# Performance work log

Hardware: AMD Instinct MI355X
Metric: run time of the kernel (lower is better)

The kernel has to match this reference:

```python
import jax, jax.numpy as jnp
import numpy as np

N_NODES = 100000
N_EDGES = 3200000
IN_DIM = 128
HIDDEN = 128
N_GRAPHS = 64


def setup_inputs() -> dict:
    key = jax.random.key(0)
    ks = jax.random.split(key, 16)
    feat = jax.random.normal(ks[0], (N_NODES, IN_DIM), dtype=jnp.float32)
    src = jax.random.randint(ks[1], (N_EDGES,), 0, N_NODES, dtype=jnp.int32)
    dst = jax.random.randint(ks[2], (N_EDGES,), 0, N_NODES, dtype=jnp.int32)
    graph_ids = jnp.sort(jax.random.randint(ks[3], (N_NODES,), 0, N_GRAPHS, dtype=jnp.int32))
    # GraphConv weights (in_feats, out_feats) + bias, DGL default glorot-ish scale
    def lin(k, fi, fo):
        s = 1.0 / np.sqrt(fi)
        kw, kb = jax.random.split(k)
        W = jax.random.uniform(kw, (fi, fo), jnp.float32, -s, s)
        b = jax.random.uniform(kb, (fo,), jnp.float32, -s, s)
        return W, b
    W1, b1 = lin(ks[4], IN_DIM, HIDDEN)
    W2, b2 = lin(ks[5], HIDDEN, HIDDEN)
    # MLPReadout(128, 1, L=3): 128->64->32->16->1
    Wm0, bm0 = lin(ks[6], 128, 64)
    Wm1, bm1 = lin(ks[7], 64, 32)
    Wm2, bm2 = lin(ks[8], 32, 16)
    Wm3, bm3 = lin(ks[9], 16, 1)
    return dict(feat=feat, src=src, dst=dst, graph_ids=graph_ids, num_graphs=N_GRAPHS,
                W1=W1, b1=b1, W2=W2, b2=b2,
                Wm0=Wm0, bm0=bm0, Wm1=Wm1, bm1=bm1, Wm2=Wm2, bm2=bm2, Wm3=Wm3, bm3=bm3)


def reference(feat, src, dst, graph_ids, num_graphs,
              W1, b1, W2, b2,
              Wm0, bm0, Wm1, bm1, Wm2, bm2, Wm3, bm3):
    N = feat.shape[0]
    ones_e = jnp.ones(src.shape[0], dtype=feat.dtype)
    # DGL GraphConv norm='both': D_out^{-1/2} on src side, D_in^{-1/2} on dst side,
    # degrees clamped to >=1 (allow_zero_in_degree=True)
    deg_out = jnp.clip(jax.ops.segment_sum(ones_e, src, num_segments=N), 1.0)
    deg_in = jnp.clip(jax.ops.segment_sum(ones_e, dst, num_segments=N), 1.0)
    norm_src = jax.lax.rsqrt(deg_out)[:, None]  # [N,1]
    norm_dst = jax.lax.rsqrt(deg_in)[:, None]

    def gconv(h, W, b):
        h = h * norm_src
        agg = jax.ops.segment_sum(h[src], dst, num_segments=N)  # SpMM: [N,d]
        return agg * norm_dst @ W + b

    h = jax.nn.relu(gconv(feat, W1, b1))
    h = jax.nn.relu(gconv(h, W2, b2))

    # dgl.mean_nodes: per-graph mean over nodes
    counts = jnp.clip(jax.ops.segment_sum(jnp.ones(N, dtype=h.dtype), graph_ids, num_segments=num_graphs), 1.0)
    hg = jax.ops.segment_sum(h, graph_ids, num_segments=num_graphs) / counts[:, None]  # [G, hidden]

    # MLPReadout
    y = jax.nn.relu(hg @ Wm0 + bm0)
    y = jax.nn.relu(y @ Wm1 + bm1)
    y = jax.nn.relu(y @ Wm2 + bm2)
    return y @ Wm3 + bm3  # [G, 1]
```

## Files before the change

### kernel.cpp

```cpp
#include <hip/hip_runtime.h>
#include <hip/hip_fp16.h>

#define N_NODES 100000
#define N_EDGES 3200000
#define DIM 128
#define NG 64
#define GS_CHUNKS 16

#define KSH 8
#define BKT 256
#define NBKT ((N_NODES + BKT - 1) / BKT)
#define CHUNK 8192
#define NBLK ((N_EDGES + CHUNK - 1) / CHUNK)

using f16x8 = __attribute__((ext_vector_type(8))) _Float16;
using f32x4 = __attribute__((ext_vector_type(4))) float;

__global__ __launch_bounds__(256) void k_hist1(const int* __restrict__ src, const int* __restrict__ dst,
                                               int* __restrict__ histD, int* __restrict__ histS,
                                               int* __restrict__ rowtot) {
    __shared__ int hD[4 * NBKT];
    __shared__ int hS[4 * NBKT];
    int t = threadIdx.x, blk = blockIdx.x;
    int w = t >> 6;
    for (int i = t; i < 4 * NBKT; i += 256) { hD[i] = 0; hS[i] = 0; }
    __syncthreads();
    int base = blk * CHUNK;
    for (int i = t; i < CHUNK; i += 256) {
        int e = base + i;
        if (e < N_EDGES) {
            atomicAdd(&hD[w * NBKT + (dst[e] >> KSH)], 1);
            atomicAdd(&hS[w * NBKT + (src[e] >> KSH)], 1);
        }
    }
    __syncthreads();
    for (int i = t; i < NBKT; i += 256) {
        int d = hD[i] + hD[NBKT + i] + hD[2 * NBKT + i] + hD[3 * NBKT + i];
        int s = hS[i] + hS[NBKT + i] + hS[2 * NBKT + i] + hS[3 * NBKT + i];
        histD[i * NBLK + blk] = d;
        histS[i * NBLK + blk] = s;
        atomicAdd(&rowtot[i], d);
        atomicAdd(&rowtot[NBKT + i], s);
    }
}

__global__ __launch_bounds__(512) void k_rowapply(int* __restrict__ histD, int* __restrict__ histS,
                                                  const int* __restrict__ rowtot) {
    __shared__ int sh[512];
    __shared__ int red[512];
    int r = blockIdx.x;
    int half = (r < NBKT) ? 0 : 1;
    int pos = half ? (r - NBKT) : r;
    int* a = half ? (histS + (size_t)pos * NBLK) : (histD + (size_t)pos * NBLK);
    int t = threadIdx.x;
    red[t] = (t < pos) ? rowtot[half * NBKT + t] : 0;
    __syncthreads();
    for (int off = 256; off > 0; off >>= 1) {
        if (t < off) red[t] += red[t + off];
        __syncthreads();
    }
    int basev = red[0];
    int x = (t < NBLK) ? a[t] : 0;
    sh[t] = x; __syncthreads();
    for (int off = 1; off < 512; off <<= 1) {
        int y = sh[t]; int u = (t >= off) ? sh[t - off] : 0;
        __syncthreads(); sh[t] = y + u; __syncthreads();
    }
    if (t < NBLK) a[t] = sh[t] - x + basev;
}

__global__ __launch_bounds__(256) void k_scatter1(const int* __restrict__ src, const int* __restrict__ dst,
                                                  const int* __restrict__ histD, const int* __restrict__ histS,
                                                  int* __restrict__ bufD, unsigned short* __restrict__ bufS) {
    __shared__ int cD[NBKT];
    __shared__ int cS[NBKT];
    int t = threadIdx.x, blk = blockIdx.x;
    for (int i = t; i < NBKT; i += 256) {
        cD[i] = histD[i * NBLK + blk];
        cS[i] = histS[i * NBLK + blk];
    }
    __syncthreads();
    int base = blk * CHUNK;
    for (int i = t; i < CHUNK; i += 256) {
        int e = base + i;
        if (e < N_EDGES) {
            int s = src[e], d = dst[e];
            int pD = atomicAdd(&cD[d >> KSH], 1);
            bufD[pD] = ((d & (BKT - 1)) << 17) | s;
            int pS = atomicAdd(&cS[s >> KSH], 1);
            bufS[pS] = (unsigned short)(s & (BKT - 1));
        }
    }
}

__global__ __launch_bounds__(256) void k_pass2s(const unsigned short* __restrict__ bufS,
                                                const int* __restrict__ histS,
                                                float* __restrict__ norm_src) {
    __shared__ int binc[BKT];
    int b = blockIdx.x, t = threadIdx.x;
    int start = histS[b * NBLK];
    int end = (b + 1 < NBKT) ? histS[(b + 1) * NBLK] : N_EDGES;
    if (t < BKT) binc[t] = 0;
    __syncthreads();
    for (int i = start + t; i < end; i += 256) atomicAdd(&binc[bufS[i]], 1);
    __syncthreads();
    int nb = N_NODES - b * BKT; if (nb > BKT) nb = BKT;
    if (t < nb) {
        int c = binc[t]; if (c < 1) c = 1;
        norm_src[b * BKT + t] = rsqrtf((float)c);
    }
}

__global__ __launch_bounds__(256) void k_pass2(const int* __restrict__ bufD,
                                               const int* __restrict__ histD,
                                               int* __restrict__ rowptr, float* __restrict__ norm_dst,
                                               int* __restrict__ col) {
    __shared__ int binc[BKT];
    __shared__ int binoff[BKT];
    int b = blockIdx.x, t = threadIdx.x;
    int start = histD[b * NBLK];
    int end = (b + 1 < NBKT) ? histD[(b + 1) * NBLK] : N_EDGES;
    if (t < BKT) binc[t] = 0;
    __syncthreads();
    for (int i = start + t; i < end; i += 256) atomicAdd(&binc[bufD[i] >> 17], 1);
    __syncthreads();
    if (t < 64) {
        int base4 = t * 4;
        int loc[4]; int s4 = 0;
        #pragma unroll
        for (int k = 0; k < 4; k++) { loc[k] = s4; s4 += binc[base4 + k]; }
        int x = s4;
        #pragma unroll
        for (int off = 1; off < 64; off <<= 1) {
            int y = __shfl_up(x, off);
            if (t >= off) x += y;
        }
        int excl = x - s4;
        #pragma unroll
        for (int k = 0; k < 4; k++) binoff[base4 + k] = excl + loc[k];
    }
    __syncthreads();
    int nb = N_NODES - b * BKT; if (nb > BKT) nb = BKT;
    if (t < nb) {
        rowptr[b * BKT + t] = start + binoff[t];
        int c = binc[t]; if (c < 1) c = 1;
        norm_dst[b * BKT + t] = rsqrtf((float)c);
    }
    if (b == NBKT - 1 && t == 0) rowptr[N_NODES] = N_EDGES;
    __syncthreads();
    if (t < BKT) binc[t] = binoff[t];
    __syncthreads();
    for (int i = start + t; i < end; i += 256) {
        int v = bufD[i];
        int ld = v >> 17, s = v & 0x1FFFF;
        int p = atomicAdd(&binc[ld], 1);
        col[start + p] = s;
    }
}

__global__ __launch_bounds__(256) void k_cast8(const float* __restrict__ in,
                                               const float* __restrict__ norm_src,
                                               unsigned* __restrict__ out) {
    int i4 = blockIdx.x * 256 + threadIdx.x;
    const int TOT = N_NODES * DIM / 4;
    if (i4 >= TOT) return;
    int row = i4 >> 5;
    float sc = norm_src[row];
    float4 v = ((const float4*)in)[i4];
    unsigned w = 0;
    w = __builtin_amdgcn_cvt_pk_fp8_f32(v.x * sc, v.y * sc, w, 0);
    w = __builtin_amdgcn_cvt_pk_fp8_f32(v.z * sc, v.w * sc, w, 1);
    out[i4] = w;
}

#define ACC8(r) do {                                                                  \
    auto p0 = __builtin_amdgcn_cvt_pk_f32_fp8((r).x, 0); a0 += p0[0]; a1 += p0[1];    \
    auto p1 = __builtin_amdgcn_cvt_pk_f32_fp8((r).x, 1); a2 += p1[0]; a3 += p1[1];    \
    auto p2 = __builtin_amdgcn_cvt_pk_f32_fp8((r).y, 0); a4 += p2[0]; a5 += p2[1];    \
    auto p3 = __builtin_amdgcn_cvt_pk_f32_fp8((r).y, 1); a6 += p3[0]; a7 += p3[1];    \
    auto p4 = __builtin_amdgcn_cvt_pk_f32_fp8((r).z, 0); a8 += p4[0]; a9 += p4[1];    \
    auto p5 = __builtin_amdgcn_cvt_pk_f32_fp8((r).z, 1); a10 += p5[0]; a11 += p5[1];  \
    auto p6 = __builtin_amdgcn_cvt_pk_f32_fp8((r).w, 0); a12 += p6[0]; a13 += p6[1];  \
    auto p7 = __builtin_amdgcn_cvt_pk_f32_fp8((r).w, 1); a14 += p7[0]; a15 += p7[1];  \
} while (0)

__global__ __launch_bounds__(256) void k_spmm8(const unsigned char* __restrict__ in,
                       const int* __restrict__ rowptr, const int* __restrict__ col,
                       const float* __restrict__ norm_dst, __half2* __restrict__ out) {
    int wid = (blockIdx.x * 256 + threadIdx.x) >> 6;
    int lane = threadIdx.x & 63;
    int rg = lane >> 3, l8 = lane & 7;
    int node = wid * 8 + rg;
    if (node >= N_NODES) return;
    int jb = rowptr[node], je = rowptr[node + 1];
    float a0 = 0.f, a1 = 0.f, a2 = 0.f, a3 = 0.f, a4 = 0.f, a5 = 0.f, a6 = 0.f, a7 = 0.f;
    float a8 = 0.f, a9 = 0.f, a10 = 0.f, a11 = 0.f, a12 = 0.f, a13 = 0.f, a14 = 0.f, a15 = 0.f;
    int j = jb;
    for (; j + 2 <= je; j += 2) {
        int s0 = col[j], s1 = col[j + 1];
        uint4 r0 = *(const uint4*)&in[(size_t)s0 * 128 + l8 * 16];
        uint4 r1 = *(const uint4*)&in[(size_t)s1 * 128 + l8 * 16];
        ACC8(r0);
        ACC8(r1);
    }
    if (j < je) {
        int s0 = col[j];
        uint4 r0 = *(const uint4*)&in[(size_t)s0 * 128 + l8 * 16];
        ACC8(r0);
    }
    float nd = norm_dst[node];
    __half2 h0 = __floats2half2_rn(a0 * nd, a1 * nd);
    __half2 h1 = __floats2half2_rn(a2 * nd, a3 * nd);
    __half2 h2 = __floats2half2_rn(a4 * nd, a5 * nd);
    __half2 h3 = __floats2half2_rn(a6 * nd, a7 * nd);
    __half2 h4 = __floats2half2_rn(a8 * nd, a9 * nd);
    __half2 h5 = __floats2half2_rn(a10 * nd, a11 * nd);
    __half2 h6 = __floats2half2_rn(a12 * nd, a13 * nd);
    __half2 h7 = __floats2half2_rn(a14 * nd, a15 * nd);
    uint4 o0, o1;
    o0.x = *(unsigned*)&h0; o0.y = *(unsigned*)&h1;
    o0.z = *(unsigned*)&h2; o0.w = *(unsigned*)&h3;
    o1.x = *(unsigned*)&h4; o1.y = *(unsigned*)&h5;
    o1.z = *(unsigned*)&h6; o1.w = *(unsigned*)&h7;
    *(uint4*)&out[(size_t)node * 64 + l8 * 8] = o0;
    *(uint4*)&out[(size_t)node * 64 + l8 * 8 + 4] = o1;
}

template <bool SCALE, bool OUT8>
__global__ __launch_bounds__(256) void k_gemm_mfma(const __half* __restrict__ A,
        const float* __restrict__ W, const float* __restrict__ bias,
        const float* __restrict__ rowscale, void* __restrict__ outp) {
    __shared__ _Float16 lds[128 * 136];
    int tid = threadIdx.x;
    for (int idx = tid * 4; idx < DIM * DIM; idx += 256 * 4) {
        int k = idx >> 7, n = idx & 127;
        float4 w = *(const float4*)&W[idx];
        lds[(n + 0) * 136 + k] = (_Float16)w.x;
        lds[(n + 1) * 136 + k] = (_Float16)w.y;
        lds[(n + 2) * 136 + k] = (_Float16)w.z;
        lds[(n + 3) * 136 + k] = (_Float16)w.w;
    }
    __syncthreads();
    int wv = tid >> 6, lane = tid & 63;
    int rbase = blockIdx.x * 64 + wv * 16;
    int l15 = lane & 15, kg = lane >> 4;
    int arow = rbase + l15; if (arow >= N_NODES) arow = N_NODES - 1;
    const _Float16* Af = (const _Float16*)A + (size_t)arow * DIM + kg * 8;
    f16x8 a0 = *(const f16x8*)(Af + 0);
    f16x8 a1 = *(const f16x8*)(Af + 32);
    f16x8 a2 = *(const f16x8*)(Af + 64);
    f16x8 a3 = *(const f16x8*)(Af + 96);
    f32x4 acc[8];
    #pragma unroll
    for (int nt = 0; nt < 8; nt++) acc[nt] = (f32x4){0.f, 0.f, 0.f, 0.f};
    #pragma unroll
    for (int nt = 0; nt < 8; nt++) {
        const _Float16* bb = &lds[(nt * 16 + l15) * 136 + kg * 8];
        f16x8 b0 = *(const f16x8*)(bb + 0);
        f16x8 b1 = *(const f16x8*)(bb + 32);
        f16x8 b2 = *(const f16x8*)(bb + 64);
        f16x8 b3 = *(const f16x8*)(bb + 96);
        acc[nt] = __builtin_amdgcn_mfma_f32_16x16x32_f16(a0, b0, acc[nt], 0, 0, 0);
        acc[nt] = __builtin_amdgcn_mfma_f32_16x16x32_f16(a1, b1, acc[nt], 0, 0, 0);
        acc[nt] = __builtin_amdgcn_mfma_f32_16x16x32_f16(a2, b2, acc[nt], 0, 0, 0);
        acc[nt] = __builtin_amdgcn_mfma_f32_16x16x32_f16(a3, b3, acc[nt], 0, 0, 0);
    }
    __syncthreads();
    float bsc[4];
    #pragma unroll
    for (int r = 0; r < 4; r++) {
        if (SCALE) {
            int row = rbase + kg * 4 + r; if (row >= N_NODES) row = N_NODES - 1;
            bsc[r] = rowscale[row];
        } else bsc[r] = 1.f;
    }
    #pragma unroll
    for (int nt = 0; nt < 8; nt++) {
        float bv = bias[nt * 16 + l15];
        #pragma unroll
        for (int r = 0; r < 4; r++) {
            float v = fmaxf(acc[nt][r] + bv, 0.f) * bsc[r];
            lds[(size_t)(wv * 16 + kg * 4 + r) * 136 + nt * 16 + l15] = (_Float16)v;
        }
    }
    __syncthreads();
    #pragma unroll
    for (int t = 0; t < 4; t++) {
        int lrow = wv * 16 + t * 4 + kg;
        int grow = rbase + t * 4 + kg;
        f16x8 v = *(const f16x8*)&lds[(size_t)lrow * 136 + l15 * 8];
        if (grow < N_NODES) {
            if (OUT8) {
                unsigned w0 = 0, w1 = 0;
                w0 = __builtin_amdgcn_cvt_pk_fp8_f32((float)v[0], (float)v[1], w0, 0);
                w0 = __builtin_amdgcn_cvt_pk_fp8_f32((float)v[2], (float)v[3], w0, 1);
                w1 = __builtin_amdgcn_cvt_pk_fp8_f32((float)v[4], (float)v[5], w1, 0);
                w1 = __builtin_amdgcn_cvt_pk_fp8_f32((float)v[6], (float)v[7], w1, 1);
                uint2 o; o.x = w0; o.y = w1;
                *(uint2*)&((unsigned char*)outp)[(size_t)grow * 128 + l15 * 8] = o;
            } else {
                *(f16x8*)&((_Float16*)outp)[(size_t)grow * DIM + l15 * 8] = v;
            }
        }
    }
}

__global__ __launch_bounds__(256) void k_graphsum_part(const __half2* __restrict__ h,
                           const int* __restrict__ gids, float* __restrict__ partial) {
    __shared__ float redx[256];
    __shared__ float redy[256];
    __shared__ int sb[2];
    int g = blockIdx.x;
    int c = blockIdx.y;
    if (threadIdx.x == 0) {
        int lo = 0, hi = N_NODES;
        while (lo < hi) { int mid = (lo + hi) >> 1; if (gids[mid] < g) lo = mid + 1; else hi = mid; }
        sb[0] = lo;
        lo = 0; hi = N_NODES;
        while (lo < hi) { int mid = (lo + hi) >> 1; if (gids[mid] <= g) lo = mid + 1; else hi = mid; }
        sb[1] = lo;
    }
    __syncthreads();
    int s = sb[0], e = sb[1];
    int p = threadIdx.x & 63;
    int r = threadIdx.x >> 6;
    int clen = (e - s + GS_CHUNKS - 1) / GS_CHUNKS;
    int b0 = s + c * clen;
    int b1 = b0 + clen; if (b1 > e) b1 = e;
    float ax = 0.f, ay = 0.f;
    for (int nd = b0 + r; nd < b1; nd += 4) {
        float2 f = __half22float2(h[(size_t)nd * 64 + p]);
        ax += f.x; ay += f.y;
    }
    redx[threadIdx.x] = ax; redy[threadIdx.x] = ay;
    __syncthreads();
    if (threadIdx.x < 64) {
        float sx = redx[threadIdx.x] + redx[threadIdx.x + 64] + redx[threadIdx.x + 128] + redx[threadIdx.x + 192];
        float sy = redy[threadIdx.x] + redy[threadIdx.x + 64] + redy[threadIdx.x + 128] + redy[threadIdx.x + 192];
        float* pp = &partial[((size_t)g * GS_CHUNKS + c) * DIM];
        pp[2 * threadIdx.x] = sx;
        pp[2 * threadIdx.x + 1] = sy;
    }
}

__global__ __launch_bounds__(128) void k_mlp(const float* __restrict__ partial,
                      const int* __restrict__ gids,
                      const float* __restrict__ Wm0, const float* __restrict__ bm0,
                      const float* __restrict__ Wm1, const float* __restrict__ bm1,
                      const float* __restrict__ Wm2, const float* __restrict__ bm2,
                      const float* __restrict__ Wm3, const float* __restrict__ bm3,
                      float* __restrict__ out) {
    __shared__ float hb[DIM];
    __shared__ float l0[64];
    __shared__ float l1[32];
    __shared__ float l2[16];
    __shared__ int scnt;
    int g = blockIdx.x;
    int t = threadIdx.x;
    if (t == 0) {
        int lo = 0, hi = N_NODES;
        while (lo < hi) { int mid = (lo + hi) >> 1; if (gids[mid] < g) lo = mid + 1; else hi = mid; }
        int s = lo;
        lo = 0; hi = N_NODES;
        while (lo < hi) { int mid = (lo + hi) >> 1; if (gids[mid] <= g) lo = mid + 1; else hi = mid; }
        int c = lo - s; if (c < 1) c = 1;
        scnt = c;
    }
    __syncthreads();
    float acc = 0.f;
    #pragma unroll
    for (int c = 0; c < GS_CHUNKS; c++)
        acc += partial[((size_t)g * GS_CHUNKS + c) * DIM + t];
    hb[t] = acc / (float)scnt;
    __syncthreads();
    if (t < 64) {
        float a = bm0[t];
        for (int k = 0; k < 128; k++) a += hb[k] * Wm0[k * 64 + t];
        l0[t] = fmaxf(a, 0.f);
    }
    __syncthreads();
    if (t < 32) {
        float a = bm1[t];
        for (int k = 0; k < 64; k++) a += l0[k] * Wm1[k * 32 + t];
        l1[t] = fmaxf(a, 0.f);
    }
    __syncthreads();
    if (t < 16) {
        float a = bm2[t];
        for (int k = 0; k < 32; k++) a += l1[k] * Wm2[k * 16 + t];
        l2[t] = fmaxf(a, 0.f);
    }
    __syncthreads();
    if (t == 0) {
        float a = bm3[0];
        for (int k = 0; k < 16; k++) a += l2[k] * Wm3[k];
        out[g] = a;
    }
}

extern "C" void kernel_launch(void* const* d_in, const int* in_sizes, int n_in,
                              void* d_out, int out_size, void* d_ws, size_t ws_size,
                              hipStream_t stream) {
    const float* feat = (const float*)d_in[0];
    const int*   src  = (const int*)d_in[1];
    const int*   dst  = (const int*)d_in[2];
    const int*   gids = (const int*)d_in[3];
    const float* W1   = (const float*)d_in[5];
    const float* b1   = (const float*)d_in[6];
    const float* W2   = (const float*)d_in[7];
    const float* b2   = (const float*)d_in[8];
    const float* Wm0  = (const float*)d_in[9];
    const float* bm0  = (const float*)d_in[10];
    const float* Wm1  = (const float*)d_in[11];
    const float* bm1  = (const float*)d_in[12];
    const float* Wm2  = (const float*)d_in[13];
    const float* bm2  = (const float*)d_in[14];
    const float* Wm3  = (const float*)d_in[15];
    const float* bm3  = (const float*)d_in[16];
    float* out = (float*)d_out;

    char* ws = (char*)d_ws;
    size_t off = 0;
    auto alloc = [&](size_t bytes) -> void* {
        void* p = ws + off;
        off += (bytes + 511) & ~(size_t)511;
        return p;
    };
    float* norm_src = (float*)alloc((size_t)N_NODES * 4);
    float* norm_dst = (float*)alloc((size_t)N_NODES * 4);
    int* rowptr   = (int*)alloc((size_t)(N_NODES + 1) * 4);
    int* histD    = (int*)alloc((size_t)NBKT * NBLK * 4);
    int* histS    = (int*)alloc((size_t)NBKT * NBLK * 4);
    int* rowtot   = (int*)alloc((size_t)(2 * NBKT) * 4);
    int* bufD     = (int*)alloc((size_t)N_EDGES * 4);
    int* colbuf   = (int*)alloc((size_t)N_EDGES * 4);
    unsigned char* feat8 = (unsigned char*)alloc((size_t)N_NODES * DIM);
    unsigned char* h8    = (unsigned char*)alloc((size_t)N_NODES * DIM);
    __half* s16   = (__half*)alloc((size_t)N_NODES * DIM * 2);
    __half* g16   = (__half*)alloc((size_t)N_NODES * DIM * 2);
    float* partial = (float*)alloc((size_t)NG * GS_CHUNKS * DIM * 4);
    unsigned short* bufS = (unsigned short*)colbuf;
    int* col = colbuf;

    hipMemsetAsync(rowtot, 0, (size_t)(2 * NBKT) * 4, stream);

    k_hist1<<<NBLK, 256, 0, stream>>>(src, dst, histD, histS, rowtot);
    k_rowapply<<<2 * NBKT, 512, 0, stream>>>(histD, histS, rowtot);
    k_scatter1<<<NBLK, 256, 0, stream>>>(src, dst, histD, histS, bufD, bufS);
    k_pass2s<<<NBKT, 256, 0, stream>>>(bufS, histS, norm_src);
    k_pass2<<<NBKT, 256, 0, stream>>>(bufD, histD, rowptr, norm_dst, col);

    k_cast8<<<(N_NODES * DIM / 4 + 255) / 256, 256, 0, stream>>>(feat, norm_src, (unsigned*)feat8);

    int sb2 = (N_NODES + 31) / 32;
    int gb = (N_NODES + 63) / 64;
    k_spmm8<<<sb2, 256, 0, stream>>>(feat8, rowptr, col, norm_dst, (__half2*)s16);
    k_gemm_mfma<true, true><<<gb, 256, 0, stream>>>(s16, W1, b1, norm_src, h8);
    k_spmm8<<<sb2, 256, 0, stream>>>(h8, rowptr, col, norm_dst, (__half2*)s16);
    k_gemm_mfma<false, false><<<gb, 256, 0, stream>>>(s16, W2, b2, nullptr, g16);

    dim3 gsg(NG, GS_CHUNKS);
    k_graphsum_part<<<gsg, 256, 0, stream>>>((const __half2*)g16, gids, partial);
    k_mlp<<<NG, 128, 0, stream>>>(partial, gids, Wm0, bm0, Wm1, bm1, Wm2, bm2, Wm3, bm3, out);
}
```

Before: 360.3 us.

## Stage bucket scatter in shared memory before coalesced global writes

The edge bucketing scatter now writes each edge into a shared-memory staging buffer at its local bucket offset. Those offsets come from a wave-level prefix scan over per-bucket counts. Each bucket's contiguous run is then copied to global memory by a full wavefront, replacing scattered per-edge global stores. This aims to cut uncoalesced write traffic, at the cost of more LDS (about 54KB, which limits occupancy), extra syncs and a serial copy loop over 391 buckets per block.

```diff
diff --git a/kernel.cpp b/kernel.cpp
--- a/kernel.cpp
+++ b/kernel.cpp
@@ -72,12 +72,45 @@
 __global__ __launch_bounds__(256) void k_scatter1(const int* __restrict__ src, const int* __restrict__ dst,
                                                   const int* __restrict__ histD, const int* __restrict__ histS,
                                                   int* __restrict__ bufD, unsigned short* __restrict__ bufS) {
-    __shared__ int cD[NBKT];
-    __shared__ int cS[NBKT];
+    __shared__ int gbD[NBKT], cntD[NBKT], offD[NBKT], curD[NBKT];
+    __shared__ int gbS[NBKT], cntS[NBKT], offS[NBKT], curS[NBKT];
+    __shared__ int stageD[CHUNK];
+    __shared__ unsigned short stageS[CHUNK];
     int t = threadIdx.x, blk = blockIdx.x;
-    for (int i = t; i < NBKT; i += 256) {
-        cD[i] = histD[i * NBLK + blk];
-        cS[i] = histS[i * NBLK + blk];
+    for (int b = t; b < NBKT; b += 256) {
+        int idx = b * NBLK + blk;
+        int st = histD[idx];
+        int nx = (idx + 1 < NBKT * NBLK) ? histD[idx + 1] : N_EDGES;
+        gbD[b] = st; cntD[b] = nx - st;
+        int st2 = histS[idx];
+        int nx2 = (idx + 1 < NBKT * NBLK) ? histS[idx + 1] : N_EDGES;
+        gbS[b] = st2; cntS[b] = nx2 - st2;
+    }
+    __syncthreads();
+    if (t < 64) {
+        int lane = t;
+        int base7 = lane * 7;
+        int loc[7]; int s7 = 0;
+        #pragma unroll
+        for (int k = 0; k < 7; k++) { int b = base7 + k; loc[k] = s7; s7 += (b < NBKT) ? cntD[b] : 0; }
+        int x = s7;
+        #pragma unroll
+        for (int off = 1; off < 64; off <<= 1) { int y = __shfl_up(x, off); if (lane >= off) x += y; }
+        int excl = x - s7;
+        #pragma unroll
+        for (int k = 0; k < 7; k++) { int b = base7 + k; if (b < NBKT) { offD[b] = excl + loc[k]; curD[b] = excl + loc[k]; } }
+    } else if (t < 128) {
+        int lane = t - 64;
+        int base7 = lane * 7;
+        int loc[7]; int s7 = 0;
+        #pragma unroll
+        for (int k = 0; k < 7; k++) { int b = base7 + k; loc[k] = s7; s7 += (b < NBKT) ? cntS[b] : 0; }
+        int x = s7;
+        #pragma unroll
+        for (int off = 1; off < 64; off <<= 1) { int y = __shfl_up(x, off); if (lane >= off) x += y; }
+        int excl = x - s7;
+        #pragma unroll
+        for (int k = 0; k < 7; k++) { int b = base7 + k; if (b < NBKT) { offS[b] = excl + loc[k]; curS[b] = excl + loc[k]; } }
     }
     __syncthreads();
     int base = blk * CHUNK;
@@ -85,11 +118,19 @@
         int e = base + i;
         if (e < N_EDGES) {
             int s = src[e], d = dst[e];
-            int pD = atomicAdd(&cD[d >> KSH], 1);
-            bufD[pD] = ((d & (BKT - 1)) << 17) | s;
-            int pS = atomicAdd(&cS[s >> KSH], 1);
-            bufS[pS] = (unsigned short)(s & (BKT - 1));
+            int pD = atomicAdd(&curD[d >> KSH], 1);
+            stageD[pD] = ((d & (BKT - 1)) << 17) | s;
+            int pS = atomicAdd(&curS[s >> KSH], 1);
+            stageS[pS] = (unsigned short)(s & (BKT - 1));
         }
+    }
+    __syncthreads();
+    int wv = t >> 6, lane = t & 63;
+    for (int b = wv; b < NBKT; b += 4) {
+        int c = cntD[b], o = offD[b], g = gbD[b];
+        for (int i = lane; i < c; i += 64) bufD[g + i] = stageD[o + i];
+        int c2 = cntS[b], o2 = offS[b], g2 = gbS[b];
+        for (int i = lane; i < c2; i += 64) bufS[g2 + i] = stageS[o2 + i];
     }
 }
 
```

Measured after the change: 351.6 us. 2.4% less time.
